# Kernel tuning notes

Hardware: AMD Instinct MI355X
Metric: run time of the kernel (lower is better)

## Reference

```python
import jax, jax.numpy as jnp
import numpy as np

ODE_UNFOLDS = 6  # keras-ncp LTCCell default
EPS = 1e-8


def setup_inputs() -> dict:
    dim = 1024
    U = 2 * dim
    B, T = 32, 128
    key = jax.random.key(0)
    ks = jax.random.split(key, 12)
    u = lambda k, shape, lo, hi: jax.random.uniform(k, shape, jnp.float32, lo, hi)
    return {
        "inputs": jax.random.normal(ks[0], (B, T, dim), jnp.float32),
        # per-neuron params (keras-ncp initializer ranges)
        "gleak": u(ks[1], (U,), 0.001, 1.0),
        "vleak": u(ks[2], (U,), -0.2, 0.2),
        "cm": u(ks[3], (U,), 0.4, 0.6),
        # per-synapse params; slot 0 = self synapse, slot 1 = pair synapse (j+dim)%U
        "w": u(ks[4], (U, 2), 0.001, 1.0),
        "sigma": u(ks[5], (U, 2), 3.0, 8.0),
        "mu": u(ks[6], (U, 2), 0.3, 0.8),
        "erev": jnp.full((U, 2), -1.0, jnp.float32),  # internal polarity -1
        # sensory synapse params; each neuron j has one sensory source j%dim
        "sens_w": u(ks[7], (U,), 0.001, 1.0),
        "sens_sigma": u(ks[8], (U,), 3.0, 8.0),
        "sens_mu": u(ks[9], (U,), 0.3, 0.8),
        "sens_erev": jnp.full((U,), 1.0, jnp.float32),  # sensory polarity +1
        # affine input/output maps (LTCCell defaults: ones / zeros)
        "input_w": jnp.ones((dim,), jnp.float32),
        "input_b": jnp.zeros((dim,), jnp.float32),
        "output_w": jnp.ones((dim,), jnp.float32),
        "output_b": jnp.zeros((dim,), jnp.float32),
    }


def reference(inputs, gleak, vleak, cm, w, sigma, mu, erev,
              sens_w, sens_sigma, sens_mu, sens_erev,
              input_w, input_b, output_w, output_b):
    B, T, dim = inputs.shape
    U = 2 * dim
    idx = jnp.arange(U)
    src_idx = jnp.stack([idx, (idx + dim) % U], axis=-1)  # [U,2] recurrent sources per dst
    smod = idx % dim                                       # sensory source per dst

    sp_w = jax.nn.softplus(w)          # [U,2]
    sp_sw = jax.nn.softplus(sens_w)    # [U]
    sp_gleak = jax.nn.softplus(gleak)  # [U]
    cm_t = jax.nn.softplus(cm) * ODE_UNFOLDS  # elapsed_time = 1.0

    def step(v, x_t):
        x = x_t * input_w + input_b                                            # [B,dim]
        s_act = sp_sw * jax.nn.sigmoid((x[:, smod] - sens_mu) * sens_sigma)    # [B,U]
        num_s = s_act * sens_erev
        den_s = s_act
        for _ in range(ODE_UNFOLDS):
            va = v[:, src_idx]                                                  # [B,U,2]
            wa = sp_w * jax.nn.sigmoid((va - mu) * sigma)                      # [B,U,2]
            num = jnp.sum(wa * erev, axis=-1) + num_s                          # [B,U]
            den = jnp.sum(wa, axis=-1) + den_s                                 # [B,U]
            v = (cm_t * v + sp_gleak * vleak + num) / (cm_t + sp_gleak + den + EPS)
        return v, None

    v0 = jnp.zeros((B, U), inputs.dtype)
    v_last, _ = jax.lax.scan(step, v0, jnp.swapaxes(inputs, 0, 1))  # scan over time
    return v_last[:, :dim] * output_w + output_b  # motor neurons + affine output map
```

## Files before the change

### kernel.cpp

```cpp
#include <hip/hip_runtime.h>

#define T_STEPS 128
#define DIM 1024
#define ODE_UNFOLDS 6
#define EPS 1e-8f
#define L2E 1.44269504088896340736f

__device__ __forceinline__ float fexp2(float x) { return __builtin_amdgcn_exp2f(x); }
__device__ __forceinline__ float frcp(float x)  { return __builtin_amdgcn_rcpf(x); }

__device__ __forceinline__ float softplus_init(float x) {
  return log2f(1.0f + exp2f(x * L2E)) * (1.0f / L2E);
}

__device__ __forceinline__ float swap_adj(float x) {
  int y = __builtin_amdgcn_mov_dpp(__float_as_int(x), 0xB1, 0xF, 0xF, true);
  return __int_as_float(y);
}

__global__ __launch_bounds__(256) void memcell_kernel(
    const float* __restrict__ inputs,
    const float* __restrict__ gleak,
    const float* __restrict__ vleak,
    const float* __restrict__ cm,
    const float* __restrict__ w,
    const float* __restrict__ sigma,
    const float* __restrict__ mu,
    const float* __restrict__ erev,
    const float* __restrict__ sens_w,
    const float* __restrict__ sens_sigma,
    const float* __restrict__ sens_mu,
    const float* __restrict__ sens_erev,
    const float* __restrict__ input_w,
    const float* __restrict__ input_b,
    const float* __restrict__ output_w,
    const float* __restrict__ output_b,
    float* __restrict__ out)
{
  const int tid  = blockIdx.x * blockDim.x + threadIdx.x;
  const int p    = tid >> 1;
  const int half = tid & 1;
  const int b    = p >> 10;
  const int col  = p & (DIM - 1);
  const int u    = col + (half << 10);

  const float spw0  = softplus_init(w[2*u]);
  const float spw1  = softplus_init(w[2*u+1]);
  const float e0    = erev[2*u];
  const float e1    = erev[2*u+1];
  const float spw0e = spw0 * e0;
  const float spw1e = spw1 * e1;
  const float sg0   = sigma[2*u],  sg1 = sigma[2*u+1];
  const float mu0   = mu[2*u],     mu1 = mu[2*u+1];
  const float negA0 = -sg0 * L2E,  B0c = mu0 * sg0 * L2E;
  const float negA1 = -sg1 * L2E,  B1c = mu1 * sg1 * L2E;
  const float gl    = softplus_init(gleak[u]);
  const float glv   = gl * vleak[u];
  const float cmt   = softplus_init(cm[u]) * (float)ODE_UNFOLDS;
  const float dbase = cmt + gl + EPS;
  const float spsw  = softplus_init(sens_w[u]);
  const float ssg   = sens_sigma[u];
  const float smu   = sens_mu[u];
  const float negAs = -ssg * L2E,  Bsc = smu * ssg * L2E;
  const float serev = sens_erev[u];
  const float iw    = input_w[col];
  const float ib    = input_b[col];

  const float* xp = inputs + ((size_t)b * T_STEPS) * DIM + col;

  float xs0 = xp[0 * DIM];
  float xs1 = xp[1 * DIM];
  float xs2 = xp[2 * DIM];
  float xs3 = xp[3 * DIM];

  float v = 0.0f;

  for (int tb = 0; tb < T_STEPS; tb += 4) {
    const float c0 = xs0, c1 = xs1, c2 = xs2, c3 = xs3;
    if (tb + 4 < T_STEPS) {
      const float* nx = xp + (size_t)(tb + 4) * DIM;
      xs0 = nx[0 * DIM];
      xs1 = nx[1 * DIM];
      xs2 = nx[2 * DIM];
      xs3 = nx[3 * DIM];
    }
    #pragma unroll
    for (int j = 0; j < 4; ++j) {
      const float xr = (j == 0) ? c0 : (j == 1) ? c1 : (j == 2) ? c2 : c3;
      const float x  = fmaf(xr, iw, ib);
      const float ts = fexp2(fmaf(x, negAs, Bsc));
      const float s  = spsw * frcp(1.0f + ts);
      const float ns = fmaf(s, serev, glv);
      const float ds = dbase + s;
      #pragma unroll
      for (int k = 0; k < ODE_UNFOLDS; ++k) {
        const float vp = swap_adj(v);
        const float t0 = fexp2(fmaf(v,  negA0, B0c));
        const float t1 = fexp2(fmaf(vp, negA1, B1c));
        const float a0 = 1.0f + t0;
        const float a1 = 1.0f + t1;
        const float D      = a0 * a1;
        const float S      = fmaf(spw0,  a1, spw1  * a0);
        const float E      = fmaf(spw0e, a1, spw1e * a0);
        const float numerN = fmaf(cmt, v, ns);
        const float nume   = fmaf(numerN, D, E);
        const float deno   = fmaf(ds, D, S);
        v = nume * frcp(deno);
      }
    }
  }

  if (half == 0) {
    out[(size_t)b * DIM + col] = fmaf(v, output_w[col], output_b[col]);
  }
}

extern "C" void kernel_launch(void* const* d_in, const int* in_sizes, int n_in,
                              void* d_out, int out_size, void* d_ws, size_t ws_size,
                              hipStream_t stream) {
  const float* inputs      = (const float*)d_in[0];
  const float* gleak       = (const float*)d_in[1];
  const float* vleak       = (const float*)d_in[2];
  const float* cm          = (const float*)d_in[3];
  const float* w           = (const float*)d_in[4];
  const float* sigma       = (const float*)d_in[5];
  const float* mu          = (const float*)d_in[6];
  const float* erev        = (const float*)d_in[7];
  const float* sens_w      = (const float*)d_in[8];
  const float* sens_sigma  = (const float*)d_in[9];
  const float* sens_mu     = (const float*)d_in[10];
  const float* sens_erev   = (const float*)d_in[11];
  const float* input_w     = (const float*)d_in[12];
  const float* input_b     = (const float*)d_in[13];
  const float* output_w    = (const float*)d_in[14];
  const float* output_b    = (const float*)d_in[15];

  const int B = in_sizes[0] / (T_STEPS * DIM);
  const int U = 2 * DIM;
  const int total_threads = B * U;
  dim3 block(256);
  dim3 grid(total_threads / 256);

  memcell_kernel<<<grid, block, 0, stream>>>(
      inputs, gleak, vleak, cm, w, sigma, mu, erev,
      sens_w, sens_sigma, sens_mu, sens_erev,
      input_w, input_b, output_w, output_b, (float*)d_out);
}
```

Baseline: 122.5 us.

## Shorten ODE dependency chain by deferring division and packing num/den math

Restructures the inner ODE recurrence so v is kept as numerator times reciprocal. The exponent arguments are computed from nume*rd with constants pre-swapped across the lane pair, so the DPP swap moves off the head of the chain and applies to the exp result instead. Numerator and denominator updates are packed into 2-wide float vectors to allow packed FMA. The sensory term for the next step is computed one step ahead and input prefetch is extended to two blocks of four. This aims to cut the serial latency per unfold, at the cost of more registers and slightly different rounding.

```diff
diff --git a/kernel.cpp b/kernel.cpp
--- a/kernel.cpp
+++ b/kernel.cpp
@@ -6,8 +6,13 @@
 #define EPS 1e-8f
 #define L2E 1.44269504088896340736f
 
+typedef float v2f __attribute__((ext_vector_type(2)));
+
 __device__ __forceinline__ float fexp2(float x) { return __builtin_amdgcn_exp2f(x); }
 __device__ __forceinline__ float frcp(float x)  { return __builtin_amdgcn_rcpf(x); }
+__device__ __forceinline__ v2f fma2(v2f a, v2f b, v2f c) {
+  return __builtin_elementwise_fma(a, b, c);
+}
 
 __device__ __forceinline__ float softplus_init(float x) {
   return log2f(1.0f + exp2f(x * L2E)) * (1.0f / L2E);
@@ -46,71 +51,81 @@
 
   const float spw0  = softplus_init(w[2*u]);
   const float spw1  = softplus_init(w[2*u+1]);
-  const float e0    = erev[2*u];
-  const float e1    = erev[2*u+1];
-  const float spw0e = spw0 * e0;
-  const float spw1e = spw1 * e1;
+  const float spw0e = spw0 * erev[2*u];
+  const float spw1e = spw1 * erev[2*u+1];
   const float sg0   = sigma[2*u],  sg1 = sigma[2*u+1];
   const float mu0   = mu[2*u],     mu1 = mu[2*u+1];
   const float negA0 = -sg0 * L2E,  B0c = mu0 * sg0 * L2E;
   const float negA1 = -sg1 * L2E,  B1c = mu1 * sg1 * L2E;
+  const float negA1x = swap_adj(negA1);
+  const float B1x    = swap_adj(B1c);
   const float gl    = softplus_init(gleak[u]);
   const float glv   = gl * vleak[u];
   const float cmt   = softplus_init(cm[u]) * (float)ODE_UNFOLDS;
   const float dbase = cmt + gl + EPS;
   const float spsw  = softplus_init(sens_w[u]);
   const float ssg   = sens_sigma[u];
-  const float smu   = sens_mu[u];
-  const float negAs = -ssg * L2E,  Bsc = smu * ssg * L2E;
+  const float negAs = -ssg * L2E,  Bsc = sens_mu[u] * ssg * L2E;
   const float serev = sens_erev[u];
   const float iw    = input_w[col];
   const float ib    = input_b[col];
+  const v2f spk1 = {spw1e, spw1};
+  const v2f spk0 = {spw0e, spw0};
+
+  auto sens = [&](float xr) -> v2f {
+    const float x  = fmaf(xr, iw, ib);
+    const float ts = fexp2(fmaf(x, negAs, Bsc));
+    const float s  = spsw * frcp(1.0f + ts);
+    v2f r; r.x = fmaf(s, serev, glv);
+    r.y = dbase + s;
+    return r;
+  };
 
   const float* xp = inputs + ((size_t)b * T_STEPS) * DIM + col;
 
-  float xs0 = xp[0 * DIM];
-  float xs1 = xp[1 * DIM];
-  float xs2 = xp[2 * DIM];
-  float xs3 = xp[3 * DIM];
+  float cur0 = xp[0 * DIM], cur1 = xp[1 * DIM], cur2 = xp[2 * DIM], cur3 = xp[3 * DIM];
+  float nxt0 = xp[4 * DIM], nxt1 = xp[5 * DIM], nxt2 = xp[6 * DIM], nxt3 = xp[7 * DIM];
 
-  float v = 0.0f;
+  v2f nd = sens(cur0);
+  float nume = 0.0f, rd = 1.0f;
 
   for (int tb = 0; tb < T_STEPS; tb += 4) {
-    const float c0 = xs0, c1 = xs1, c2 = xs2, c3 = xs3;
-    if (tb + 4 < T_STEPS) {
-      const float* nx = xp + (size_t)(tb + 4) * DIM;
-      xs0 = nx[0 * DIM];
-      xs1 = nx[1 * DIM];
-      xs2 = nx[2 * DIM];
-      xs3 = nx[3 * DIM];
+    float l0 = 0.f, l1 = 0.f, l2 = 0.f, l3 = 0.f;
+    const bool more = (tb + 8) < T_STEPS;
+    if (more) {
+      const float* nx = xp + (size_t)(tb + 8) * DIM;
+      l0 = nx[0 * DIM]; l1 = nx[1 * DIM]; l2 = nx[2 * DIM]; l3 = nx[3 * DIM];
     }
     #pragma unroll
     for (int j = 0; j < 4; ++j) {
-      const float xr = (j == 0) ? c0 : (j == 1) ? c1 : (j == 2) ? c2 : c3;
-      const float x  = fmaf(xr, iw, ib);
-      const float ts = fexp2(fmaf(x, negAs, Bsc));
-      const float s  = spsw * frcp(1.0f + ts);
-      const float ns = fmaf(s, serev, glv);
-      const float ds = dbase + s;
+      const float xn = (j == 0) ? cur1 : (j == 1) ? cur2 : (j == 2) ? cur3 : nxt0;
+      const v2f nd_next = sens(xn);
       #pragma unroll
       for (int k = 0; k < ODE_UNFOLDS; ++k) {
-        const float vp = swap_adj(v);
-        const float t0 = fexp2(fmaf(v,  negA0, B0c));
-        const float t1 = fexp2(fmaf(vp, negA1, B1c));
-        const float a0 = 1.0f + t0;
-        const float a1 = 1.0f + t1;
-        const float D      = a0 * a1;
-        const float S      = fmaf(spw0,  a1, spw1  * a0);
-        const float E      = fmaf(spw0e, a1, spw1e * a0);
-        const float numerN = fmaf(cmt, v, ns);
-        const float nume   = fmaf(numerN, D, E);
-        const float deno   = fmaf(ds, D, S);
-        v = nume * frcp(deno);
+        const float nnc  = nume * negA1x;
+        const float nn0  = nume * negA0;
+        const float tc   = fexp2(fmaf(nnc, rd, B1x));
+        const float t0   = fexp2(fmaf(nn0, rd, B0c));
+        const float v    = nume * rd;
+        const float t1   = swap_adj(tc);
+        v2f a; a.x = t0; a.y = t1;
+        a = a + 1.0f;
+        const float D = a.x * a.y;
+        v2f P = spk1 * a.x;
+        P = fma2(spk0, (v2f){a.y, a.y}, P);
+        v2f q; q.x = fmaf(cmt, v, nd.x); q.y = nd.y;
+        const v2f ND = fma2(q, (v2f){D, D}, P);
+        nume = ND.x;
+        rd   = frcp(ND.y);
       }
+      nd = nd_next;
     }
+    cur0 = nxt0; cur1 = nxt1; cur2 = nxt2; cur3 = nxt3;
+    if (more) { nxt0 = l0; nxt1 = l1; nxt2 = l2; nxt3 = l3; }
   }
 
   if (half == 0) {
+    const float v = nume * rd;
     out[(size_t)b * DIM + col] = fmaf(v, output_w[col], output_b[col]);
   }
 }
```

New measurement: 124.9 us. No clear change (+2.0%).
